# Kernel optimization log

Measured on AMD Instinct MI355X. Metric: run time of the kernel, lower is better.

The kernel has to match this reference:

```python
import jax, jax.numpy as jnp
import numpy as np

EPS = 1e-12


def _pchip_slopes(y, x):
    """PCHIP (Fritsch-Carlson) slopes. y: (S, K), x: (K) -> (S, K)."""
    K = y.shape[-1]
    if K < 2:
        return jnp.zeros_like(y)
    h = x[1:] - x[:-1]                              # (K-1,)
    delta = (y[..., 1:] - y[..., :-1]) / (h + EPS)  # (S, K-1)
    if K == 2:
        return jnp.broadcast_to(delta[..., :1], y.shape).astype(y.dtype)
    # interior slopes: weighted harmonic mean where secants agree in sign
    delta_prev = delta[..., :-1]
    delta_next = delta[..., 1:]
    same_sign = delta_prev * delta_next > 0
    h_prev = h[:-1]
    h_next = h[1:]
    w1 = 2.0 * h_next + h_prev
    w2 = h_next + 2.0 * h_prev
    denom = w1 / (delta_prev + EPS) + w2 / (delta_next + EPS)
    d_int = (w1 + w2) / (denom + EPS)
    d_mid = jnp.where(same_sign, d_int, jnp.zeros_like(d_int))  # (S, K-2)
    # left endpoint (one-sided, shape-limited)
    h0, h1 = h[0], h[1]
    delta0 = delta[..., 0]
    delta1 = delta[..., 1]
    d0 = ((2.0 * h0 + h1) * delta0 - h0 * delta1) / (h0 + h1 + EPS)
    d0 = jnp.where(jnp.sign(d0) != jnp.sign(delta0), jnp.zeros_like(d0), d0)
    d0 = jnp.where((jnp.sign(delta0) != jnp.sign(delta1)) & (jnp.abs(d0) > 3.0 * jnp.abs(delta0)), 3.0 * delta0, d0)
    # right endpoint
    hn1, hn2 = h[-1], h[-2]
    deltan1 = delta[..., -1]
    deltan2 = delta[..., -2]
    dn = ((2.0 * hn1 + hn2) * deltan1 - hn1 * deltan2) / (hn1 + hn2 + EPS)
    dn = jnp.where(jnp.sign(dn) != jnp.sign(deltan1), jnp.zeros_like(dn), dn)
    dn = jnp.where((jnp.sign(deltan1) != jnp.sign(deltan2)) & (jnp.abs(dn) > 3.0 * jnp.abs(deltan1)), 3.0 * deltan1, dn)
    return jnp.concatenate([d0[..., None], d_mid, dn[..., None]], axis=-1)


def setup_inputs() -> dict:
    key = jax.random.key(0)
    k1, k2 = jax.random.split(key)
    B, S, K = 4096, 4096, 64
    x_min, x_max = -3.0, 3.0
    xq = jax.random.normal(k1, (B, S), dtype=jnp.float32) * 2.0  # some queries outside domain
    coeffs = jax.random.normal(k2, (S, K), dtype=jnp.float32)
    knots = jnp.linspace(x_min, x_max, K, dtype=jnp.float32)
    return {"xq": xq, "coeffs": coeffs, "knots": knots}


def reference(xq, coeffs, knots):
    y = coeffs                                   # (S, K)
    d = _pchip_slopes(y, knots)                  # (S, K)
    K = knots.shape[0]
    x0_dom = knots[0]
    x1_dom = knots[-1]
    below = xq < x0_dom
    above = xq > x1_dom
    xq_c = jnp.clip(xq, x0_dom, x1_dom)
    idx = jnp.searchsorted(knots, xq_c) - 1      # (B, S) interval index
    idx = jnp.clip(idx, 0, K - 2)
    x0 = knots[idx]
    x1 = knots[idx + 1]
    h = x1 - x0 + EPS
    t = (xq_c - x0) / h
    t2 = t * t
    t3 = t2 * t
    h00 = 2.0 * t3 - 3.0 * t2 + 1.0
    h10 = t3 - 2.0 * t2 + t
    h01 = -2.0 * t3 + 3.0 * t2
    h11 = t3 - t2
    s_idx = jnp.arange(y.shape[0])[None, :]      # (1, S) spline index
    y0 = y[s_idx, idx]
    y1 = y[s_idx, idx + 1]
    d0 = d[s_idx, idx]
    d1 = d[s_idx, idx + 1]
    interp = h00 * y0 + h10 * h * d0 + h01 * y1 + h11 * h * d1
    out = jnp.where(below, y[None, :, 0] + d[None, :, 0] * (xq - x0_dom), interp)
    out = jnp.where(above, y[None, :, -1] + d[None, :, -1] * (xq - x1_dom), out)
    return out
```

## Files before the change

### kernel.cpp

```cpp
#include <hip/hip_runtime.h>

#define EPSF 1e-12f

__device__ __forceinline__ float sgnf(float x) {
    return (x > 0.f) ? 1.f : ((x < 0.f) ? -1.f : 0.f);
}

__global__ void pchip_slopes_kernel(const float* __restrict__ coeffs,
                                    const float* __restrict__ knots,
                                    float2* __restrict__ yd,
                                    int S, int K) {
    int s = blockIdx.x;
    int k = threadIdx.x;
    __shared__ float skn[64];
    __shared__ float sy[64];
    __shared__ float sh[64];
    __shared__ float sdel[64];

    float y = coeffs[s * K + k];
    sy[k] = y;
    skn[k] = knots[k];
    __syncthreads();
    if (k < K - 1) {
        float h = skn[k + 1] - skn[k];
        sh[k] = h;
        sdel[k] = (sy[k + 1] - sy[k]) / (h + EPSF);
    }
    __syncthreads();

    float d;
    if (k == 0) {
        float h0 = sh[0], h1 = sh[1];
        float de0 = sdel[0], de1 = sdel[1];
        d = ((2.f * h0 + h1) * de0 - h0 * de1) / (h0 + h1 + EPSF);
        if (sgnf(d) != sgnf(de0)) d = 0.f;
        if ((sgnf(de0) != sgnf(de1)) && (fabsf(d) > 3.f * fabsf(de0))) d = 3.f * de0;
    } else if (k == K - 1) {
        float hn1 = sh[K - 2], hn2 = sh[K - 3];
        float dn1 = sdel[K - 2], dn2 = sdel[K - 3];
        d = ((2.f * hn1 + hn2) * dn1 - hn1 * dn2) / (hn1 + hn2 + EPSF);
        if (sgnf(d) != sgnf(dn1)) d = 0.f;
        if ((sgnf(dn1) != sgnf(dn2)) && (fabsf(d) > 3.f * fabsf(dn1))) d = 3.f * dn1;
    } else {
        float dp = sdel[k - 1], dn = sdel[k];
        float hp = sh[k - 1], hn = sh[k];
        bool same = dp * dn > 0.f;
        float w1 = 2.f * hn + hp;
        float w2 = hn + 2.f * hp;
        float denom = w1 / (dp + EPSF) + w2 / (dn + EPSF);
        float dint = (w1 + w2) / (denom + EPSF);
        d = same ? dint : 0.f;
    }
    yd[(size_t)s * K + k] = make_float2(sy[k], d);
}

#define STILE 64
__global__ __launch_bounds__(256) void pchip_eval_tiled(
    const float* __restrict__ xq,
    const float2* __restrict__ yd,
    const float* __restrict__ knots,
    float* __restrict__ out,
    int S, int K, int b_chunk)
{
    __shared__ float2 tile[STILE * 65];

    int s0 = blockIdx.x * STILE;
    int b0 = blockIdx.y * b_chunk;
    int tid = threadIdx.x;
    int stride = K + 1;

    for (int t = tid; t < STILE * K; t += 256) {
        int sl = t >> 6;
        int k  = t & 63;
        tile[sl * stride + k] = yd[(size_t)(s0 + sl) * K + k];
    }
    float x0d = knots[0];
    float x1d = knots[K - 1];
    float invh = (float)(K - 1) / (x1d - x0d);
    __syncthreads();

    int wave = tid >> 6;
    int lane = tid & 63;
    const float2* row = tile + lane * stride;

    for (int it = wave; it < b_chunk; it += 4) {
        size_t off = (size_t)(b0 + it) * S + s0 + lane;
        float x = xq[off];

        float xc = fminf(fmaxf(x, x0d), x1d);
        float tf = (xc - x0d) * invh;
        int idx = (int)tf;
        idx = min(idx, K - 2);
        float t = tf - (float)idx;
        float h = 1.0f / invh + EPSF;

        float2 p0 = row[idx];
        float2 p1 = row[idx + 1];

        float t2 = t * t;
        float t3 = t2 * t;
        float h00 = 2.f * t3 - 3.f * t2 + 1.f;
        float h10 = t3 - 2.f * t2 + t;
        float h01 = -2.f * t3 + 3.f * t2;
        float h11 = t3 - t2;
        float res = h00 * p0.x + h10 * h * p0.y + h01 * p1.x + h11 * h * p1.y;
        if (x < x0d) res = p0.x + p0.y * (x - x0d);
        if (x > x1d) res = p1.x + p1.y * (x - x1d);

        out[off] = res;
    }
}

extern "C" void kernel_launch(void* const* d_in, const int* in_sizes, int n_in,
                              void* d_out, int out_size, void* d_ws, size_t ws_size,
                              hipStream_t stream) {
    const float* xq     = (const float*)d_in[0];
    const float* coeffs = (const float*)d_in[1];
    const float* knots  = (const float*)d_in[2];
    float* out = (float*)d_out;

    int K = in_sizes[2];
    int S = in_sizes[1] / K;
    int N = in_sizes[0];
    int B = N / S;

    float2* yd = (float2*)d_ws;

    pchip_slopes_kernel<<<S, K, 0, stream>>>(coeffs, knots, yd, S, K);

    int n_btiles = 16;
    int b_chunk = B / n_btiles;
    dim3 grid(S / STILE, n_btiles);
    pchip_eval_tiled<<<grid, 256, 0, stream>>>(xq, yd, knots, out, S, K, b_chunk);
}
```

Measured before the change: 139.3 us.

## Fuse PCHIP slope computation into eval kernel with batched row loads

```diff
diff --git a/kernel.cpp b/kernel.cpp
--- a/kernel.cpp
+++ b/kernel.cpp
@@ -1,113 +1,119 @@
 #include <hip/hip_runtime.h>
 
 #define EPSF 1e-12f
+#define STILE 64
+#define KK 64
+#define LSTR 65
 
 __device__ __forceinline__ float sgnf(float x) {
     return (x > 0.f) ? 1.f : ((x < 0.f) ? -1.f : 0.f);
 }
 
-__global__ void pchip_slopes_kernel(const float* __restrict__ coeffs,
-                                    const float* __restrict__ knots,
-                                    float2* __restrict__ yd,
-                                    int S, int K) {
-    int s = blockIdx.x;
-    int k = threadIdx.x;
-    __shared__ float skn[64];
-    __shared__ float sy[64];
-    __shared__ float sh[64];
-    __shared__ float sdel[64];
+__global__ __launch_bounds__(256) void pchip_fused(
+    const float* __restrict__ xq,
+    const float* __restrict__ coeffs,
+    const float* __restrict__ knots,
+    float* __restrict__ out,
+    int S, int b_chunk)
+{
+    __shared__ float yp[STILE * LSTR];
+    __shared__ float dpl[STILE * LSTR];
+    __shared__ float skn[KK];
 
-    float y = coeffs[s * K + k];
-    sy[k] = y;
-    skn[k] = knots[k];
+    int tid = threadIdx.x;
+    int s0 = blockIdx.x * STILE;
+    int b0 = blockIdx.y * b_chunk;
+
+    if (tid < KK) skn[tid] = knots[tid];
+    for (int t = tid; t < STILE * KK; t += 256) {
+        int sl = t >> 6, k = t & 63;
+        yp[sl * LSTR + k] = coeffs[(size_t)(s0 + sl) * KK + k];
+    }
     __syncthreads();
-    if (k < K - 1) {
-        float h = skn[k + 1] - skn[k];
-        sh[k] = h;
-        sdel[k] = (sy[k + 1] - sy[k]) / (h + EPSF);
+    for (int t = tid; t < STILE * KK; t += 256) {
+        int sl = t >> 6, k = t & 63;
+        if (k < KK - 1) {
+            float h = skn[k + 1] - skn[k];
+            dpl[sl * LSTR + k] = (yp[sl * LSTR + k + 1] - yp[sl * LSTR + k]) / (h + EPSF);
+        }
+    }
+    __syncthreads();
+    float dreg[16];
+#pragma unroll
+    for (int i = 0; i < 16; i++) {
+        int t = tid + i * 256;
+        int sl = t >> 6, k = t & 63;
+        const float* del = dpl + sl * LSTR;
+        float d;
+        if (k == 0) {
+            float h0 = skn[1] - skn[0], h1 = skn[2] - skn[1];
+            float de0 = del[0], de1 = del[1];
+            d = ((2.f * h0 + h1) * de0 - h0 * de1) / (h0 + h1 + EPSF);
+            if (sgnf(d) != sgnf(de0)) d = 0.f;
+            if ((sgnf(de0) != sgnf(de1)) && (fabsf(d) > 3.f * fabsf(de0))) d = 3.f * de0;
+        } else if (k == KK - 1) {
+            float hn1 = skn[KK - 1] - skn[KK - 2], hn2 = skn[KK - 2] - skn[KK - 3];
+            float dn1 = del[KK - 2], dn2 = del[KK - 3];
+            d = ((2.f * hn1 + hn2) * dn1 - hn1 * dn2) / (hn1 + hn2 + EPSF);
+            if (sgnf(d) != sgnf(dn1)) d = 0.f;
+            if ((sgnf(dn1) != sgnf(dn2)) && (fabsf(d) > 3.f * fabsf(dn1))) d = 3.f * dn1;
+        } else {
+            float dprev = del[k - 1], dnext = del[k];
+            float hp = skn[k] - skn[k - 1], hn = skn[k + 1] - skn[k];
+            bool same = dprev * dnext > 0.f;
+            float w1 = 2.f * hn + hp;
+            float w2 = hn + 2.f * hp;
+            float denom = w1 / (dprev + EPSF) + w2 / (dnext + EPSF);
+            float dint = (w1 + w2) / (denom + EPSF);
+            d = same ? dint : 0.f;
+        }
+        dreg[i] = d;
+    }
+    __syncthreads();
+#pragma unroll
+    for (int i = 0; i < 16; i++) {
+        int t = tid + i * 256;
+        int sl = t >> 6, k = t & 63;
+        dpl[sl * LSTR + k] = dreg[i];
     }
     __syncthreads();
 
-    float d;
-    if (k == 0) {
-        float h0 = sh[0], h1 = sh[1];
-        float de0 = sdel[0], de1 = sdel[1];
-        d = ((2.f * h0 + h1) * de0 - h0 * de1) / (h0 + h1 + EPSF);
-        if (sgnf(d) != sgnf(de0)) d = 0.f;
-        if ((sgnf(de0) != sgnf(de1)) && (fabsf(d) > 3.f * fabsf(de0))) d = 3.f * de0;
-    } else if (k == K - 1) {
-        float hn1 = sh[K - 2], hn2 = sh[K - 3];
-        float dn1 = sdel[K - 2], dn2 = sdel[K - 3];
-        d = ((2.f * hn1 + hn2) * dn1 - hn1 * dn2) / (hn1 + hn2 + EPSF);
-        if (sgnf(d) != sgnf(dn1)) d = 0.f;
-        if ((sgnf(dn1) != sgnf(dn2)) && (fabsf(d) > 3.f * fabsf(dn1))) d = 3.f * dn1;
-    } else {
-        float dp = sdel[k - 1], dn = sdel[k];
-        float hp = sh[k - 1], hn = sh[k];
-        bool same = dp * dn > 0.f;
-        float w1 = 2.f * hn + hp;
-        float w2 = hn + 2.f * hp;
-        float denom = w1 / (dp + EPSF) + w2 / (dn + EPSF);
-        float dint = (w1 + w2) / (denom + EPSF);
-        d = same ? dint : 0.f;
-    }
-    yd[(size_t)s * K + k] = make_float2(sy[k], d);
-}
+    float x0d = skn[0], x1d = skn[KK - 1];
+    float invh = (float)(KK - 1) / (x1d - x0d);
+    float huni = 1.0f / invh + EPSF;
+    int wave = tid >> 6, lane = tid & 63;
+    const float* yrow = yp + lane * LSTR;
+    const float* drow = dpl + lane * LSTR;
 
-#define STILE 64
-__global__ __launch_bounds__(256) void pchip_eval_tiled(
-    const float* __restrict__ xq,
-    const float2* __restrict__ yd,
-    const float* __restrict__ knots,
-    float* __restrict__ out,
-    int S, int K, int b_chunk)
-{
-    __shared__ float2 tile[STILE * 65];
-
-    int s0 = blockIdx.x * STILE;
-    int b0 = blockIdx.y * b_chunk;
-    int tid = threadIdx.x;
-    int stride = K + 1;
-
-    for (int t = tid; t < STILE * K; t += 256) {
-        int sl = t >> 6;
-        int k  = t & 63;
-        tile[sl * stride + k] = yd[(size_t)(s0 + sl) * K + k];
-    }
-    float x0d = knots[0];
-    float x1d = knots[K - 1];
-    float invh = (float)(K - 1) / (x1d - x0d);
-    __syncthreads();
-
-    int wave = tid >> 6;
-    int lane = tid & 63;
-    const float2* row = tile + lane * stride;
-
-    for (int it = wave; it < b_chunk; it += 4) {
-        size_t off = (size_t)(b0 + it) * S + s0 + lane;
-        float x = xq[off];
-
-        float xc = fminf(fmaxf(x, x0d), x1d);
-        float tf = (xc - x0d) * invh;
-        int idx = (int)tf;
-        idx = min(idx, K - 2);
-        float t = tf - (float)idx;
-        float h = 1.0f / invh + EPSF;
-
-        float2 p0 = row[idx];
-        float2 p1 = row[idx + 1];
-
-        float t2 = t * t;
-        float t3 = t2 * t;
-        float h00 = 2.f * t3 - 3.f * t2 + 1.f;
-        float h10 = t3 - 2.f * t2 + t;
-        float h01 = -2.f * t3 + 3.f * t2;
-        float h11 = t3 - t2;
-        float res = h00 * p0.x + h10 * h * p0.y + h01 * p1.x + h11 * h * p1.y;
-        if (x < x0d) res = p0.x + p0.y * (x - x0d);
-        if (x > x1d) res = p1.x + p1.y * (x - x1d);
-
-        out[off] = res;
+    int rows_per_wave = b_chunk >> 2;
+    int base = b0 + wave * rows_per_wave;
+    for (int ii = 0; ii < rows_per_wave; ii += 4) {
+        size_t off0 = (size_t)(base + ii) * S + s0 + lane;
+        float xv[4];
+#pragma unroll
+        for (int j = 0; j < 4; j++) xv[j] = xq[off0 + (size_t)j * S];
+        float rv[4];
+#pragma unroll
+        for (int j = 0; j < 4; j++) {
+            float x = xv[j];
+            float xc = fminf(fmaxf(x, x0d), x1d);
+            float tf = (xc - x0d) * invh;
+            int idx = min((int)tf, KK - 2);
+            float t = tf - (float)idx;
+            float y0 = yrow[idx], y1 = yrow[idx + 1];
+            float d0 = drow[idx], d1 = drow[idx + 1];
+            float t2 = t * t, t3 = t2 * t;
+            float h00 = 2.f * t3 - 3.f * t2 + 1.f;
+            float h10 = t3 - 2.f * t2 + t;
+            float h01 = -2.f * t3 + 3.f * t2;
+            float h11 = t3 - t2;
+            float res = h00 * y0 + h10 * huni * d0 + h01 * y1 + h11 * huni * d1;
+            if (x < x0d) res = y0 + d0 * (x - x0d);
+            if (x > x1d) res = y1 + d1 * (x - x1d);
+            rv[j] = res;
+        }
+#pragma unroll
+        for (int j = 0; j < 4; j++) out[off0 + (size_t)j * S] = rv[j];
     }
 }
 
@@ -124,12 +130,8 @@
     int N = in_sizes[0];
     int B = N / S;
 
-    float2* yd = (float2*)d_ws;
-
-    pchip_slopes_kernel<<<S, K, 0, stream>>>(coeffs, knots, yd, S, K);
-
     int n_btiles = 16;
     int b_chunk = B / n_btiles;
     dim3 grid(S / STILE, n_btiles);
-    pchip_eval_tiled<<<grid, 256, 0, stream>>>(xq, yd, knots, out, S, K, b_chunk);
+    pchip_fused<<<grid, 256, 0, stream>>>(xq, coeffs, knots, out, S, b_chunk);
 }
```

Result: no change. 136.9 us (-1.7%).
